# Kernel optimization log

Measured on AMD Instinct MI355X. Metric: run time of the kernel, lower is better.

Reference implementation:

```python
import jax, jax.numpy as jnp
import numpy as np

M, K, N, GROUP = 4096, 4096, 14336, 64


def setup_inputs() -> dict:
    key = jax.random.key(0)
    k1, k2, k3 = jax.random.split(key, 3)
    x = jax.random.normal(k1, (M, K), dtype=jnp.float32)
    # int4 quantized weight values in [0, 15], symmetric around zero-point 8
    q_weight = jax.random.randint(k2, (K, N), 0, 16, dtype=jnp.int32)
    # per-group scales: one scale per GROUP rows of k, per output column
    scales = jax.random.uniform(k3, (K // GROUP, N), dtype=jnp.float32) * 0.02
    return {"x": x, "q_weight": q_weight, "scales": scales, "group_size": GROUP}


def reference(x, q_weight, scales, group_size):
    # Marlin int4 GEMM math (act_order=False): dequantize per k-group, then GEMM.
    k, n = q_weight.shape
    g = k // group_size
    # (q - 8) * scale, scale broadcast over each group of `group_size` k-rows
    w = (q_weight.reshape(g, group_size, n).astype(scales.dtype) - 8.0) * scales[:, None, :]
    w = w.reshape(k, n)  # [K, N] dequantized weight
    return x @ w  # [M, N]
```

## Files before the change

kernel.cpp:

```cpp
#include <hip/hip_runtime.h>

#define MDIM 4096
#define KDIM 4096
#define NDIM 14336

typedef __attribute__((ext_vector_type(8))) short bf16x8;
typedef __attribute__((ext_vector_type(4))) short bf16x4;
typedef __attribute__((ext_vector_type(4))) float f32x4;

__device__ __forceinline__ unsigned short f2bf(float f) {
  unsigned u = __float_as_uint(f);
  return (unsigned short)((u + 0x7FFFu + ((u >> 16) & 1u)) >> 16);
}

__device__ __forceinline__ void async_copy16(const void* g, void* l) {
  __builtin_amdgcn_global_load_lds((const __attribute__((address_space(1))) unsigned*)g,
                                   (__attribute__((address_space(3))) unsigned*)l, 16, 0, 0);
}

__global__ __launch_bounds__(256) void cvt_x_kernel(const float* __restrict__ X,
                                                    short* __restrict__ Xb) {
  const int i = blockIdx.x * 256 + threadIdx.x;
  const float4* p = (const float4*)X + (size_t)i * 2;
  const float4 a = p[0], b = p[1];
  bf16x8 v;
  v[0] = f2bf(a.x); v[1] = f2bf(a.y); v[2] = f2bf(a.z); v[3] = f2bf(a.w);
  v[4] = f2bf(b.x); v[5] = f2bf(b.y); v[6] = f2bf(b.z); v[7] = f2bf(b.w);
  *((bf16x8*)Xb + i) = v;
}

constexpr int TPD = 76;
__global__ __launch_bounds__(256) void dequant_w_kernel(const int* __restrict__ Q,
                                                        const float* __restrict__ S,
                                                        short* __restrict__ Wt) {
  __shared__ short Ls[64 * TPD];
  const int k0 = blockIdx.x * 64;
  const int n0 = blockIdx.y * 64;
  const int t  = threadIdx.x;
  const int g  = k0 >> 6;

  const int n4 = (t & 15) * 4;
  const int rb = (t >> 4) * 4;
  const float4 s4 = *(const float4*)(S + (size_t)g * NDIM + n0 + n4);
  int4 q[4];
#pragma unroll
  for (int i = 0; i < 4; ++i)
    q[i] = *(const int4*)(Q + (size_t)(k0 + rb + i) * NDIM + n0 + n4);
  {
    bf16x4 v;
    v[0] = (short)f2bf((float)(q[0].x - 8) * s4.x);
    v[1] = (short)f2bf((float)(q[1].x - 8) * s4.x);
    v[2] = (short)f2bf((float)(q[2].x - 8) * s4.x);
    v[3] = (short)f2bf((float)(q[3].x - 8) * s4.x);
    *(bf16x4*)&Ls[(n4 + 0) * TPD + rb] = v;
    v[0] = (short)f2bf((float)(q[0].y - 8) * s4.y);
    v[1] = (short)f2bf((float)(q[1].y - 8) * s4.y);
    v[2] = (short)f2bf((float)(q[2].y - 8) * s4.y);
    v[3] = (short)f2bf((float)(q[3].y - 8) * s4.y);
    *(bf16x4*)&Ls[(n4 + 1) * TPD + rb] = v;
    v[0] = (short)f2bf((float)(q[0].z - 8) * s4.z);
    v[1] = (short)f2bf((float)(q[1].z - 8) * s4.z);
    v[2] = (short)f2bf((float)(q[2].z - 8) * s4.z);
    v[3] = (short)f2bf((float)(q[3].z - 8) * s4.z);
    *(bf16x4*)&Ls[(n4 + 2) * TPD + rb] = v;
    v[0] = (short)f2bf((float)(q[0].w - 8) * s4.w);
    v[1] = (short)f2bf((float)(q[1].w - 8) * s4.w);
    v[2] = (short)f2bf((float)(q[2].w - 8) * s4.w);
    v[3] = (short)f2bf((float)(q[3].w - 8) * s4.w);
    *(bf16x4*)&Ls[(n4 + 3) * TPD + rb] = v;
  }
  __syncthreads();

  const int nr = t >> 2;
  const int kc = (t & 3) * 16;
  const short* lr = &Ls[nr * TPD + kc];
  bf16x4 a0 = *(const bf16x4*)(lr + 0);
  bf16x4 a1 = *(const bf16x4*)(lr + 4);
  bf16x4 a2 = *(const bf16x4*)(lr + 8);
  bf16x4 a3 = *(const bf16x4*)(lr + 12);
  bf16x8 v0, v1;
#pragma unroll
  for (int j = 0; j < 4; ++j) { v0[j] = a0[j]; v0[4 + j] = a1[j]; v1[j] = a2[j]; v1[4 + j] = a3[j]; }
  short* wp = Wt + (size_t)(n0 + nr) * KDIM + k0 + kc;
  *(bf16x8*)wp = v0;
  *(bf16x8*)(wp + 8) = v1;
}

__global__ __launch_bounds__(256, 2)
void gemm_bf16tt(const short* __restrict__ Xb, const short* __restrict__ Wt,
                 float* __restrict__ Out) {
  __shared__ short As[128 * 64];
  __shared__ short Bs[128 * 64];

  const int bm = blockIdx.x * 128;
  const int bn = blockIdx.y * 128;
  const int tid = threadIdx.x, lane = tid & 63, wave = tid >> 6;
  const int wm = (wave & 1) * 64, wn = (wave >> 1) * 64;
  const int quad = lane >> 4, l16 = lane & 15;
  const int lx = l16 & 7;

  f32x4 acc[4][4];
#pragma unroll
  for (int i = 0; i < 4; ++i)
#pragma unroll
    for (int j = 0; j < 4; ++j) acc[i][j] = (f32x4){0.f, 0.f, 0.f, 0.f};

  const int row0 = tid >> 3;
  const int kof  = (((tid & 7) ^ (row0 & 7))) * 8;
  const size_t aoff = (size_t)(bm + row0) * KDIM + kof;
  const size_t boff = (size_t)(bn + row0) * KDIM + kof;
  short* const la = &As[(wave * 64) * 8];
  short* const lb = &Bs[(wave * 64) * 8];

  for (int kt = 0; kt < KDIM / 64; ++kt) {
    const int k0 = kt * 64;
    __syncthreads();
#pragma unroll
    for (int p = 0; p < 4; ++p) {
      async_copy16(Xb + aoff + (size_t)p * 32 * KDIM + k0, la + p * 2048);
      async_copy16(Wt + boff + (size_t)p * 32 * KDIM + k0, lb + p * 2048);
    }
    __syncthreads();

#pragma unroll
    for (int kk = 0; kk < 64; kk += 32) {
      const int sbase = kk >> 3;
      bf16x8 af[4], bfr[4];
#pragma unroll
      for (int i = 0; i < 4; ++i)
        af[i] = *(const bf16x8*)&As[(wm + i * 16 + l16) * 64 + (((sbase + quad) ^ lx) << 3)];
#pragma unroll
      for (int j = 0; j < 4; ++j)
        bfr[j] = *(const bf16x8*)&Bs[(wn + j * 16 + l16) * 64 + (((sbase + quad) ^ lx) << 3)];
#pragma unroll
      for (int i = 0; i < 4; ++i)
#pragma unroll
        for (int j = 0; j < 4; ++j)
          acc[i][j] = __builtin_amdgcn_mfma_f32_16x16x32_bf16(af[i], bfr[j], acc[i][j], 0, 0, 0);
    }
  }

#pragma unroll
  for (int i = 0; i < 4; ++i) {
    const int r0 = bm + wm + i * 16 + quad * 4;
#pragma unroll
    for (int j = 0; j < 4; ++j) {
      const int col = bn + wn + j * 16 + l16;
#pragma unroll
      for (int r = 0; r < 4; ++r)
        Out[(size_t)(r0 + r) * NDIM + col] = acc[i][j][r];
    }
  }
}

constexpr int BKP = 72;
__global__ __launch_bounds__(256, 2)
void marlin_int4_gemm(const float* __restrict__ X, const int* __restrict__ Q,
                      const float* __restrict__ S, float* __restrict__ Out) {
  __shared__ short As[128 * BKP];
  __shared__ short Bs[128 * BKP];
  const int bm = blockIdx.x * 128, bn = blockIdx.y * 128;
  const int tid = threadIdx.x, lane = tid & 63, wave = tid >> 6;
  const int wm = (wave & 1) * 64, wn = (wave >> 1) * 64;
  const int quad = lane >> 4, l16 = lane & 15;
  const int nB = tid & 127, krB = (tid >> 7) * 32;
  f32x4 acc[4][4];
#pragma unroll
  for (int i = 0; i < 4; ++i)
#pragma unroll
    for (int j = 0; j < 4; ++j) acc[i][j] = (f32x4){0.f, 0.f, 0.f, 0.f};
  for (int kt = 0; kt < KDIM / 64; ++kt) {
    const int k0 = kt * 64;
    const float s = S[kt * NDIM + bn + nB];
    const float bias = -8.0f * s;
    __syncthreads();
#pragma unroll
    for (int i = 0; i < 8; ++i) {
      const int idx4 = tid + (i << 8);
      const int row = idx4 >> 4, col = (idx4 & 15) << 2;
      const float4 v = *(const float4*)(X + (size_t)(bm + row) * KDIM + k0 + col);
      ushort4 b;
      b.x = f2bf(v.x); b.y = f2bf(v.y); b.z = f2bf(v.z); b.w = f2bf(v.w);
      *(ushort4*)(&As[row * BKP + col]) = b;
    }
    unsigned short wb[32];
#pragma unroll
    for (int j = 0; j < 32; ++j) {
      const int qv = Q[(size_t)(k0 + krB + j) * NDIM + bn + nB];
      wb[j] = f2bf((float)qv * s + bias);
    }
    {
      short* brow = &Bs[nB * BKP + krB];
#pragma unroll
      for (int c = 0; c < 4; ++c) {
        bf16x8 v;
#pragma unroll
        for (int e = 0; e < 8; ++e) v[e] = (short)wb[c * 8 + e];
        *(bf16x8*)(brow + c * 8) = v;
      }
    }
    __syncthreads();
#pragma unroll
    for (int kk = 0; kk < 64; kk += 32) {
      bf16x8 af[4], bfr[4];
#pragma unroll
      for (int i = 0; i < 4; ++i)
        af[i] = *(const bf16x8*)&As[(wm + i * 16 + l16) * BKP + kk + quad * 8];
#pragma unroll
      for (int j = 0; j < 4; ++j)
        bfr[j] = *(const bf16x8*)&Bs[(wn + j * 16 + l16) * BKP + kk + quad * 8];
#pragma unroll
      for (int i = 0; i < 4; ++i)
#pragma unroll
        for (int j = 0; j < 4; ++j)
          acc[i][j] = __builtin_amdgcn_mfma_f32_16x16x32_bf16(af[i], bfr[j], acc[i][j], 0, 0, 0);
    }
  }
#pragma unroll
  for (int i = 0; i < 4; ++i) {
    const int r0 = bm + wm + i * 16 + quad * 4;
#pragma unroll
    for (int j = 0; j < 4; ++j) {
      const int col = bn + wn + j * 16 + l16;
#pragma unroll
      for (int r = 0; r < 4; ++r)
        Out[(size_t)(r0 + r) * NDIM + col] = acc[i][j][r];
    }
  }
}

extern "C" void kernel_launch(void* const* d_in, const int* in_sizes, int n_in,
                              void* d_out, int out_size, void* d_ws, size_t ws_size,
                              hipStream_t stream) {
  const float* X = (const float*)d_in[0];
  const int*   Q = (const int*)d_in[1];
  const float* S = (const float*)d_in[2];
  float* Out = (float*)d_out;

  const size_t xb_elems = (size_t)MDIM * KDIM;
  const size_t wt_elems = (size_t)NDIM * KDIM;
  const size_t need = (xb_elems + wt_elems) * sizeof(short);

  if (ws_size >= need) {
    short* Xb = (short*)d_ws;
    short* Wt = Xb + xb_elems;
    cvt_x_kernel<<<(int)(xb_elems / 8 / 256), 256, 0, stream>>>(X, Xb);
    dequant_w_kernel<<<dim3(KDIM / 64, NDIM / 64), 256, 0, stream>>>(Q, S, Wt);
    gemm_bf16tt<<<dim3(MDIM / 128, NDIM / 128), 256, 0, stream>>>(Xb, Wt, Out);
  } else {
    marlin_int4_gemm<<<dim3(MDIM / 128, NDIM / 128), 256, 0, stream>>>(X, Q, S, Out);
  }
}
```

Baseline: 843.1 us.

## Double-buffer LDS tiles, enlarge GEMM block to 256x128 with grid swizzle

The bf16 GEMM now uses 512 threads per block computing a 256x128 tile, and double-buffers the A and B LDS tiles. The next k-tile's async global-to-LDS copies are issued before the MFMAs on the current tile, and a block-index swizzle is meant to improve L2 reuse. This aims to overlap memory latency with compute and to cut barriers per iteration. It uses more LDS per block (96KB) and drops to one block per CU. Correctness depends on the single barrier being enough to order the async LDS writes, which is unclear without an explicit vmcnt wait.

```diff
diff --git a/kernel.cpp b/kernel.cpp
--- a/kernel.cpp
+++ b/kernel.cpp
@@ -86,16 +86,20 @@
   *(bf16x8*)(wp + 8) = v1;
 }
 
-__global__ __launch_bounds__(256, 2)
+__global__ __launch_bounds__(512, 1)
 void gemm_bf16tt(const short* __restrict__ Xb, const short* __restrict__ Wt,
                  float* __restrict__ Out) {
-  __shared__ short As[128 * 64];
-  __shared__ short Bs[128 * 64];
-
-  const int bm = blockIdx.x * 128;
-  const int bn = blockIdx.y * 128;
+  __shared__ short As[2][256 * 64];
+  __shared__ short Bs[2][128 * 64];
+
+  const int lin = blockIdx.y * gridDim.x + blockIdx.x;
+  const int swz = (lin & 7) * 224 + (lin >> 3);
+  const int bm = (swz & 15) * 256;
+  const int bn = (swz >> 4) * 128;
+
   const int tid = threadIdx.x, lane = tid & 63, wave = tid >> 6;
-  const int wm = (wave & 1) * 64, wn = (wave >> 1) * 64;
+  const int wm = (wave >> 1) * 64;
+  const int wn = (wave & 1) * 64;
   const int quad = lane >> 4, l16 = lane & 15;
   const int lx = l16 & 7;
 
@@ -106,39 +110,50 @@
     for (int j = 0; j < 4; ++j) acc[i][j] = (f32x4){0.f, 0.f, 0.f, 0.f};
 
   const int row0 = tid >> 3;
-  const int kof  = (((tid & 7) ^ (row0 & 7))) * 8;
+  const int kof  = ((tid & 7) ^ (row0 & 7)) * 8;
   const size_t aoff = (size_t)(bm + row0) * KDIM + kof;
   const size_t boff = (size_t)(bn + row0) * KDIM + kof;
-  short* const la = &As[(wave * 64) * 8];
-  short* const lb = &Bs[(wave * 64) * 8];
+  short* const la[2] = {&As[0][(wave * 8) * 64], &As[1][(wave * 8) * 64]};
+  short* const lb[2] = {&Bs[0][(wave * 8) * 64], &Bs[1][(wave * 8) * 64]};
+
+#define STAGE(buf, k0)                                                              \
+  do {                                                                              \
+    _Pragma("unroll") for (int p = 0; p < 4; ++p)                                   \
+        async_copy16(Xb + aoff + (size_t)p * 64 * KDIM + (k0), la[buf] + p * 4096); \
+    _Pragma("unroll") for (int p = 0; p < 2; ++p)                                   \
+        async_copy16(Wt + boff + (size_t)p * 64 * KDIM + (k0), lb[buf] + p * 4096); \
+  } while (0)
+
+  STAGE(0, 0);
+  __syncthreads();
 
   for (int kt = 0; kt < KDIM / 64; ++kt) {
-    const int k0 = kt * 64;
-    __syncthreads();
-#pragma unroll
-    for (int p = 0; p < 4; ++p) {
-      async_copy16(Xb + aoff + (size_t)p * 32 * KDIM + k0, la + p * 2048);
-      async_copy16(Wt + boff + (size_t)p * 32 * KDIM + k0, lb + p * 2048);
-    }
-    __syncthreads();
-
+    const int cur = kt & 1;
+    if (kt + 1 < KDIM / 64) {
+      if (cur) STAGE(0, (kt + 1) * 64);
+      else     STAGE(1, (kt + 1) * 64);
+    }
+    const short* Ab = As[cur];
+    const short* Bb = Bs[cur];
 #pragma unroll
     for (int kk = 0; kk < 64; kk += 32) {
       const int sbase = kk >> 3;
       bf16x8 af[4], bfr[4];
 #pragma unroll
       for (int i = 0; i < 4; ++i)
-        af[i] = *(const bf16x8*)&As[(wm + i * 16 + l16) * 64 + (((sbase + quad) ^ lx) << 3)];
+        af[i] = *(const bf16x8*)&Ab[(wm + i * 16 + l16) * 64 + (((sbase + quad) ^ lx) << 3)];
 #pragma unroll
       for (int j = 0; j < 4; ++j)
-        bfr[j] = *(const bf16x8*)&Bs[(wn + j * 16 + l16) * 64 + (((sbase + quad) ^ lx) << 3)];
+        bfr[j] = *(const bf16x8*)&Bb[(wn + j * 16 + l16) * 64 + (((sbase + quad) ^ lx) << 3)];
 #pragma unroll
       for (int i = 0; i < 4; ++i)
 #pragma unroll
         for (int j = 0; j < 4; ++j)
           acc[i][j] = __builtin_amdgcn_mfma_f32_16x16x32_bf16(af[i], bfr[j], acc[i][j], 0, 0, 0);
     }
-  }
+    __syncthreads();
+  }
+#undef STAGE
 
 #pragma unroll
   for (int i = 0; i < 4; ++i) {
@@ -246,7 +261,7 @@
     short* Wt = Xb + xb_elems;
     cvt_x_kernel<<<(int)(xb_elems / 8 / 256), 256, 0, stream>>>(X, Xb);
     dequant_w_kernel<<<dim3(KDIM / 64, NDIM / 64), 256, 0, stream>>>(Q, S, Wt);
-    gemm_bf16tt<<<dim3(MDIM / 128, NDIM / 128), 256, 0, stream>>>(Xb, Wt, Out);
+    gemm_bf16tt<<<dim3(MDIM / 256, NDIM / 128), 512, 0, stream>>>(Xb, Wt, Out);
   } else {
     marlin_int4_gemm<<<dim3(MDIM / 128, NDIM / 128), 256, 0, stream>>>(X, Q, S, Out);
   }
```

After: 1.039 ms. 1.23x slower.
